# Kernel optimization log

Measured on AMD Instinct MI355X. Metric: run time of the kernel, lower is better.

The kernel has to match this reference:

```python
import jax, jax.numpy as jnp
import numpy as np

D = 1024      # in_dim
HS = 64       # head_size
H = 16        # num_heads
B, S = 2, 2048


def setup_inputs() -> dict:
    key = jax.random.key(0)
    k1, k2, k3, k4, k5, k6 = jax.random.split(key, 6)
    scale = 1.0 / np.sqrt(D)
    x = jax.random.normal(k1, (B, S, D), dtype=jnp.float32)
    # Stacked per-head projection weights (torch Linear weight is [out,in];
    # random init so layout only needs to be consistent). query weight exists
    # in the torch module but is never used (source bug), so it is omitted.
    Wk = jax.random.normal(k2, (H, D, HS), dtype=jnp.float32) * scale
    Wv = jax.random.normal(k3, (H, D, HS), dtype=jnp.float32) * scale
    Wproj = jax.random.normal(k4, (H * HS, D), dtype=jnp.float32) * (1.0 / np.sqrt(H * HS))
    bproj = jax.random.normal(k5, (D,), dtype=jnp.float32) * 0.01
    return {"x": x, "Wk": Wk, "Wv": Wv, "Wproj": Wproj, "bproj": bproj}


def reference(x, Wk, Wv, Wproj, bproj):
    # Faithful to source: k = key(x); q = value(x); v = value(x)  (q == v, no softmax)
    k = jnp.einsum("bsd,hde->bhse", x, Wk)   # [B,H,S,HS]
    v = jnp.einsum("bsd,hde->bhse", x, Wv)   # [B,H,S,HS]
    q = v
    inv_sqrt = jnp.asarray(HS, x.dtype) ** -0.5
    wei = jnp.einsum("bhse,bhte->bhst", q, k) * inv_sqrt  # [B,H,S,S], unnormalized
    out = jnp.einsum("bhst,bhte->bhse", wei, v)            # [B,H,S,HS]
    # concat heads: [B,S,H*HS]
    out = jnp.transpose(out, (0, 2, 1, 3)).reshape(x.shape[0], x.shape[1], H * HS)
    return out @ Wproj + bproj  # [B,S,D]
```

## Files before the change

kernel.cpp:

```cpp
#include <hip/hip_runtime.h>

#define B_ 2
#define S_ 2048
#define D_ 1024
#define H_ 16
#define HS_ 64
#define HD_ 1024
#define BS_ (B_*S_)
#define BK_ 128
#define BKO_ 128
#define TP_ 136

typedef __attribute__((ext_vector_type(8))) short short8_t;
typedef __attribute__((ext_vector_type(4))) float float4_t;

__device__ inline unsigned short f32_to_bf16(float f) {
  unsigned int u = __float_as_uint(f);
  u += 0x7FFF + ((u >> 16) & 1);
  return (unsigned short)(u >> 16);
}

__device__ inline void async_copy16(const void* g, void* lds) {
  __builtin_amdgcn_global_load_lds(
      (const __attribute__((address_space(1))) void*)g,
      (__attribute__((address_space(3))) void*)lds, 16, 0, 0);
}


__global__ __launch_bounds__(256) void prep_kernel(
    const float* __restrict__ x, const float* __restrict__ Wk,
    const float* __restrict__ Wv, unsigned short* __restrict__ xb,
    unsigned short* __restrict__ Wkvt) {
  const int blk = blockIdx.x;
  const int tid = threadIdx.x;
  __shared__ float lds[64][65];
  if (blk < 4096) {
    int idx = blk * 256 + tid;
    float4 v = ((const float4*)x)[idx];
    ushort4 o;
    o.x = f32_to_bf16(v.x); o.y = f32_to_bf16(v.y);
    o.z = f32_to_bf16(v.z); o.w = f32_to_bf16(v.w);
    ((ushort4*)xb)[idx] = o;
    return;
  }
  const int wblk = blk - 4096;
  const int h = wblk >> 4;
  const int d0 = (wblk & 15) * 64;
#pragma unroll
  for (int i = 0; i < 16; ++i) {
    int idx = tid + i * 256; int dd = idx >> 6, e = idx & 63;
    lds[e][dd] = Wk[((size_t)h * D_ + d0 + dd) * HS_ + e];
  }
  __syncthreads();
#pragma unroll
  for (int i = 0; i < 16; ++i) {
    int idx = tid + i * 256; int e = idx >> 6, dd = idx & 63;
    Wkvt[((size_t)h * 128 + e) * D_ + d0 + dd] = f32_to_bf16(lds[e][dd]);
  }
  __syncthreads();
#pragma unroll
  for (int i = 0; i < 16; ++i) {
    int idx = tid + i * 256; int dd = idx >> 6, e = idx & 63;
    lds[e][dd] = Wv[((size_t)h * D_ + d0 + dd) * HS_ + e];
  }
  __syncthreads();
#pragma unroll
  for (int i = 0; i < 16; ++i) {
    int idx = tid + i * 256; int e = idx >> 6, dd = idx & 63;
    Wkvt[((size_t)h * 128 + 64 + e) * D_ + d0 + dd] = f32_to_bf16(lds[e][dd]);
  }
}

__global__ __launch_bounds__(256) void kv_mfma_kernel(
    const unsigned short* __restrict__ xb,
    const unsigned short* __restrict__ Wkvt,
    unsigned short* __restrict__ Vb,
    float* __restrict__ Mpart) {
  const int blk = blockIdx.x;
  const int stile = blk & 31;
  const int h = blk >> 5;
  const int s0 = stile * 128;
  const int tid = threadIdx.x;
  const int lane = tid & 63;
  const int wid = tid >> 6;
  const int wm = wid & 1, wn = wid >> 1;
  const int quad = lane >> 4, l16 = lane & 15;
  const int srow4 = lane >> 4;
  const int xa = l16 & 7;

  __shared__ __align__(16) unsigned char smem[2 * 128 * BK_ * 2];
  unsigned short* As  = (unsigned short*)smem;
  unsigned short* Bs  = (unsigned short*)(smem + 128 * BK_ * 2);
  unsigned short* Ktl = (unsigned short*)smem;
  unsigned short* Vtl = (unsigned short*)(smem + 64 * TP_ * 2);

  float4_t acc[4][4];
  const float4_t fz = {0.f, 0.f, 0.f, 0.f};
#pragma unroll
  for (int i = 0; i < 4; ++i)
#pragma unroll
    for (int j = 0; j < 4; ++j) acc[i][j] = fz;

  for (int k0 = 0; k0 < D_; k0 += BK_) {
#pragma unroll
    for (int i = 0; i < 8; ++i) {
      int g = wid * 8 + i;
      int r = g * 4 + srow4;
      int ch = ((lane & 15) ^ (r & 7)) * 8;
      async_copy16(xb + (size_t)(s0 + r) * D_ + k0 + ch, As + g * 4 * BK_);
      async_copy16(Wkvt + ((size_t)h * 128 + r) * D_ + k0 + ch, Bs + g * 4 * BK_);
    }
    __syncthreads();
#pragma unroll
    for (int ks = 0; ks < 4; ++ks) {
      short8_t a[4], b[4];
#pragma unroll
      for (int mi = 0; mi < 4; ++mi)
        a[mi] = *(const short8_t*)(As + (wm * 64 + mi * 16 + l16) * BK_ +
                                   ((ks * 4 + quad) ^ xa) * 8);
#pragma unroll
      for (int ni = 0; ni < 4; ++ni)
        b[ni] = *(const short8_t*)(Bs + (wn * 64 + ni * 16 + l16) * BK_ +
                                   ((ks * 4 + quad) ^ xa) * 8);
#pragma unroll
      for (int mi = 0; mi < 4; ++mi)
#pragma unroll
        for (int ni = 0; ni < 4; ++ni)
          acc[mi][ni] = __builtin_amdgcn_mfma_f32_16x16x32_bf16(
              a[mi], b[ni], acc[mi][ni], 0, 0, 0);
    }
    __syncthreads();
  }

  {
    unsigned short* dstT = (wn == 0) ? Ktl : Vtl;
#pragma unroll
    for (int mi = 0; mi < 4; ++mi)
#pragma unroll
      for (int ni = 0; ni < 4; ++ni) {
        int f = ni * 16 + l16;
        int sm = wm * 64 + mi * 16 + quad * 4;
        ushort4 o;
        o.x = f32_to_bf16(acc[mi][ni][0]);
        o.y = f32_to_bf16(acc[mi][ni][1]);
        o.z = f32_to_bf16(acc[mi][ni][2]);
        o.w = f32_to_bf16(acc[mi][ni][3]);
        *(ushort4*)&dstT[f * TP_ + sm] = o;
      }
  }
  __syncthreads();

#pragma unroll
  for (int u = 0; u < 4; ++u) {
    int unit = tid + u * 256;
    int s = unit & 127;
    int ec = (unit >> 7) * 8;
    union { unsigned short u16[8]; uint4 v; } t;
#pragma unroll
    for (int e = 0; e < 8; ++e) t.u16[e] = Vtl[(ec + e) * TP_ + s];
    *(uint4*)&Vb[(size_t)(s0 + s) * HD_ + h * 64 + ec] = t.v;
  }

  {
    float4_t macc[4];
#pragma unroll
    for (int ni = 0; ni < 4; ++ni) macc[ni] = fz;
#pragma unroll
    for (int ss = 0; ss < 4; ++ss) {
      short8_t ka = *(const short8_t*)&Ktl[(wid * 16 + l16) * TP_ + ss * 32 + quad * 8];
#pragma unroll
      for (int ni = 0; ni < 4; ++ni) {
        short8_t vv = *(const short8_t*)&Vtl[(ni * 16 + l16) * TP_ + ss * 32 + quad * 8];
        macc[ni] = __builtin_amdgcn_mfma_f32_16x16x32_bf16(ka, vv, macc[ni], 0, 0, 0);
      }
    }
    float* mdst = Mpart + ((size_t)stile * H_ + h) * 4096;
#pragma unroll
    for (int ni = 0; ni < 4; ++ni) {
      int e = ni * 16 + l16;
#pragma unroll
      for (int r = 0; r < 4; ++r) {
        int f = wid * 16 + quad * 4 + r;
        mdst[f * 64 + e] = macc[ni][r];
      }
    }
  }
}

__global__ __launch_bounds__(256) void m_reduce_kernel(
    const float* __restrict__ Mpart, float* __restrict__ M) {
  const int gid = blockIdx.x * 256 + threadIdx.x;
  const int e0 = gid * 4;
  const int bh = e0 >> 12;
  const int idx = e0 & 4095;
  const int b = bh >> 4, h = bh & 15;
  float4 s = {0.f, 0.f, 0.f, 0.f};
#pragma unroll
  for (int p = 0; p < 16; ++p) {
    const float4 v =
        *(const float4*)&Mpart[(((size_t)(b * 16 + p)) * H_ + h) * 4096 + idx];
    s.x += v.x; s.y += v.y; s.z += v.z; s.w += v.w;
  }
  s.x *= 0.125f; s.y *= 0.125f; s.z *= 0.125f; s.w *= 0.125f;
  *(float4*)&M[(size_t)bh * 4096 + idx] = s;
}

__global__ __launch_bounds__(256) void p_kernel(
    const float* __restrict__ M, const float* __restrict__ Wproj,
    unsigned short* __restrict__ Pt) {
  const int blk = blockIdx.x;
  const int dtile = blk & 15;
  const int h = (blk >> 4) & 15;
  const int b = blk >> 8;
  const int d0 = dtile * 64;
  const int tid = threadIdx.x;
  const int tx = tid & 15, ty = tid >> 4;
  __shared__ float Ms[64][68];
  __shared__ float Ws[64][68];
  const size_t mbase = ((size_t)(b * H_ + h)) * HS_ * HS_;
#pragma unroll
  for (int i = 0; i < 16; ++i) {
    int idx = tid + i * 256;
    int f = idx >> 6, e = idx & 63;
    Ms[e][f] = M[mbase + idx];
    Ws[f][e] = Wproj[(size_t)(h * HS_ + f) * D_ + d0 + e];
  }
  __syncthreads();
  float acc[4][4] = {};
#pragma unroll
  for (int kk = 0; kk < 64; ++kk) {
    const float4 a4 = *(const float4*)&Ms[kk][ty * 4];
    const float4 b4 = *(const float4*)&Ws[kk][tx * 4];
    const float a[4] = {a4.x, a4.y, a4.z, a4.w};
    const float bb[4] = {b4.x, b4.y, b4.z, b4.w};
#pragma unroll
    for (int i = 0; i < 4; ++i)
#pragma unroll
      for (int j = 0; j < 4; ++j) acc[i][j] += a[i] * bb[j];
  }
  __syncthreads();
#pragma unroll
  for (int i = 0; i < 4; ++i)
#pragma unroll
    for (int j = 0; j < 4; ++j)
      Ms[tx * 4 + j][ty * 4 + i] = acc[i][j];
  __syncthreads();
  {
    int c = tid >> 2, ch = tid & 3;
    unsigned short* dst = Pt + ((size_t)(b * D_ + d0 + c)) * HD_ + h * 64 + ch * 16;
#pragma unroll
    for (int e = 0; e < 16; ++e) dst[e] = f32_to_bf16(Ms[c][ch * 16 + e]);
  }
}

__global__ __launch_bounds__(256) void out_mfma_kernel(
    const unsigned short* __restrict__ Vb,
    const unsigned short* __restrict__ Pt,
    const float* __restrict__ bproj,
    float* __restrict__ out) {
  const int blk = blockIdx.x;
  const int ntile = blk & 15;
  const int stile = blk >> 4;
  const int s0 = stile * 128;
  const int n0 = ntile * 64;
  const int b = s0 >> 11;
  const int tid = threadIdx.x;
  const int lane = tid & 63;
  const int wid = tid >> 6;
  const int wm = wid & 1, wn = wid >> 1;
  const int quad = lane >> 4, l16 = lane & 15;
  const int srow4 = lane >> 4;
  const int xa = l16 & 7;

  __shared__ __align__(16) unsigned short As[128 * BKO_];
  __shared__ __align__(16) unsigned short Bs[64 * BKO_];

  float4_t acc[4][2];
  const float4_t fz = {0.f, 0.f, 0.f, 0.f};
#pragma unroll
  for (int i = 0; i < 4; ++i)
#pragma unroll
    for (int j = 0; j < 2; ++j) acc[i][j] = fz;

  const unsigned short* Bpanel = Pt + (size_t)b * D_ * HD_;
  for (int k0 = 0; k0 < HD_; k0 += BKO_) {
#pragma unroll
    for (int i = 0; i < 8; ++i) {
      int g = wid * 8 + i;
      int r = g * 4 + srow4;
      int ch = ((lane & 15) ^ (r & 7)) * 8;
      async_copy16(Vb + (size_t)(s0 + r) * HD_ + k0 + ch, As + g * 4 * BKO_);
    }
#pragma unroll
    for (int i = 0; i < 4; ++i) {
      int g = wid * 4 + i;
      int r = g * 4 + srow4;
      int ch = ((lane & 15) ^ (r & 7)) * 8;
      async_copy16(Bpanel + (size_t)(n0 + r) * HD_ + k0 + ch, Bs + g * 4 * BKO_);
    }
    __syncthreads();
    short8_t a[4][4], bfr[2][4];
#pragma unroll
    for (int mi = 0; mi < 4; ++mi)
#pragma unroll
      for (int ks = 0; ks < 4; ++ks)
        a[mi][ks] = *(const short8_t*)(As + (wm * 64 + mi * 16 + l16) * BKO_ +
                                       ((ks * 4 + quad) ^ xa) * 8);
#pragma unroll
    for (int ni = 0; ni < 2; ++ni)
#pragma unroll
      for (int ks = 0; ks < 4; ++ks)
        bfr[ni][ks] = *(const short8_t*)(Bs + (wn * 32 + ni * 16 + l16) * BKO_ +
                                         ((ks * 4 + quad) ^ xa) * 8);
#pragma unroll
    for (int ks = 0; ks < 4; ++ks)
#pragma unroll
      for (int mi = 0; mi < 4; ++mi)
#pragma unroll
        for (int ni = 0; ni < 2; ++ni)
          acc[mi][ni] = __builtin_amdgcn_mfma_f32_16x16x32_bf16(
              a[mi][ks], bfr[ni][ks], acc[mi][ni], 0, 0, 0);
    __syncthreads();
  }
#pragma unroll
  for (int ni = 0; ni < 2; ++ni) {
    int col = n0 + wn * 32 + ni * 16 + l16;
    float bias = bproj[col];
#pragma unroll
    for (int mi = 0; mi < 4; ++mi) {
      int rowb = s0 + wm * 64 + mi * 16 + quad * 4;
#pragma unroll
      for (int r = 0; r < 4; ++r)
        out[(size_t)(rowb + r) * D_ + col] = acc[mi][ni][r] + bias;
    }
  }
}

extern "C" void kernel_launch(void* const* d_in, const int* in_sizes, int n_in,
                              void* d_out, int out_size, void* d_ws, size_t ws_size,
                              hipStream_t stream) {
  const float* x = (const float*)d_in[0];
  const float* Wk = (const float*)d_in[1];
  const float* Wv = (const float*)d_in[2];
  const float* Wproj = (const float*)d_in[3];
  const float* bproj = (const float*)d_in[4];
  float* out = (float*)d_out;

  char* ws = (char*)d_ws;
  unsigned short* xb = (unsigned short*)ws;
  unsigned short* Wkvt = xb + (size_t)BS_ * D_;
  unsigned short* Vb = Wkvt + (size_t)H_ * 128 * D_;
  float* Mpart = (float*)(Vb + (size_t)BS_ * HD_);
  float* M = Mpart + (size_t)32 * H_ * 4096;
  unsigned short* Pt = (unsigned short*)(M + (size_t)B_ * H_ * 4096);

  prep_kernel<<<dim3(4096 + H_ * (D_ / 64)), dim3(256), 0, stream>>>(x, Wk, Wv, xb, Wkvt);
  kv_mfma_kernel<<<dim3(32 * H_), dim3(256), 0, stream>>>(xb, Wkvt, Vb, Mpart);
  m_reduce_kernel<<<dim3(128), dim3(256), 0, stream>>>(Mpart, M);
  p_kernel<<<dim3(B_ * H_ * (D_ / 64)), dim3(256), 0, stream>>>(M, Wproj, Pt);
  out_mfma_kernel<<<dim3(32 * 16), dim3(256), 0, stream>>>(Vb, Pt, bproj, out);
}
```

Baseline: 132.1 us.

## Double-buffer LDS K-tiles with async prefetch in projection GEMM kernels

Both the KV projection and output projection GEMMs now use a two-stage LDS ping-pong with K-step 64 instead of a single buffer with K-step 128. The next tile's global_load_lds is issued before computing the current tile, using explicit vmcnt waits and raw barriers so loads overlap with MFMA work. s_setprio is raised around the MFMA blocks. This adds LDS usage (64KB in the KV kernel), which may cut occupancy, and relies on hand-counted vmcnt values being correct.

```diff
diff --git a/kernel.cpp b/kernel.cpp
--- a/kernel.cpp
+++ b/kernel.cpp
@@ -7,8 +7,7 @@
 #define HS_ 64
 #define HD_ 1024
 #define BS_ (B_*S_)
-#define BK_ 128
-#define BKO_ 128
+#define KS_ 64
 #define TP_ 136
 
 typedef __attribute__((ext_vector_type(8))) short short8_t;
@@ -85,12 +84,15 @@
   const int wid = tid >> 6;
   const int wm = wid & 1, wn = wid >> 1;
   const int quad = lane >> 4, l16 = lane & 15;
-  const int srow4 = lane >> 4;
+  const int srow8 = lane >> 3;
+  const int sc8 = lane & 7;
   const int xa = l16 & 7;
 
-  __shared__ __align__(16) unsigned char smem[2 * 128 * BK_ * 2];
-  unsigned short* As  = (unsigned short*)smem;
-  unsigned short* Bs  = (unsigned short*)(smem + 128 * BK_ * 2);
+  __shared__ __align__(16) unsigned char smem[65536];
+  unsigned short* const A0 = (unsigned short*)smem;
+  unsigned short* const B0 = (unsigned short*)(smem + 16384);
+  unsigned short* const A1 = (unsigned short*)(smem + 32768);
+  unsigned short* const B1 = (unsigned short*)(smem + 49152);
   unsigned short* Ktl = (unsigned short*)smem;
   unsigned short* Vtl = (unsigned short*)(smem + 64 * TP_ * 2);
 
@@ -101,35 +103,56 @@
 #pragma unroll
     for (int j = 0; j < 4; ++j) acc[i][j] = fz;
 
-  for (int k0 = 0; k0 < D_; k0 += BK_) {
-#pragma unroll
-    for (int i = 0; i < 8; ++i) {
-      int g = wid * 8 + i;
-      int r = g * 4 + srow4;
-      int ch = ((lane & 15) ^ (r & 7)) * 8;
-      async_copy16(xb + (size_t)(s0 + r) * D_ + k0 + ch, As + g * 4 * BK_);
-      async_copy16(Wkvt + ((size_t)h * 128 + r) * D_ + k0 + ch, Bs + g * 4 * BK_);
-    }
-    __syncthreads();
-#pragma unroll
-    for (int ks = 0; ks < 4; ++ks) {
+  auto stage = [&](int kt, unsigned short* Ad, unsigned short* Bd) {
+    const int k0 = kt * KS_;
+#pragma unroll
+    for (int i = 0; i < 4; ++i) {
+      int g = wid * 4 + i;
+      int r = g * 8 + srow8;
+      int ch = (sc8 ^ (r & 7)) * 8;
+      async_copy16(xb + (size_t)(s0 + r) * D_ + k0 + ch, Ad + g * 8 * KS_);
+      async_copy16(Wkvt + ((size_t)h * 128 + r) * D_ + k0 + ch, Bd + g * 8 * KS_);
+    }
+  };
+  auto compute = [&](const unsigned short* Ac, const unsigned short* Bc) {
+#pragma unroll
+    for (int ks = 0; ks < 2; ++ks) {
       short8_t a[4], b[4];
 #pragma unroll
       for (int mi = 0; mi < 4; ++mi)
-        a[mi] = *(const short8_t*)(As + (wm * 64 + mi * 16 + l16) * BK_ +
+        a[mi] = *(const short8_t*)(Ac + (wm * 64 + mi * 16 + l16) * KS_ +
                                    ((ks * 4 + quad) ^ xa) * 8);
 #pragma unroll
       for (int ni = 0; ni < 4; ++ni)
-        b[ni] = *(const short8_t*)(Bs + (wn * 64 + ni * 16 + l16) * BK_ +
+        b[ni] = *(const short8_t*)(Bc + (wn * 64 + ni * 16 + l16) * KS_ +
                                    ((ks * 4 + quad) ^ xa) * 8);
+      __builtin_amdgcn_s_setprio(1);
 #pragma unroll
       for (int mi = 0; mi < 4; ++mi)
 #pragma unroll
         for (int ni = 0; ni < 4; ++ni)
           acc[mi][ni] = __builtin_amdgcn_mfma_f32_16x16x32_bf16(
               a[mi], b[ni], acc[mi][ni], 0, 0, 0);
-    }
-    __syncthreads();
+      __builtin_amdgcn_s_setprio(0);
+    }
+  };
+
+  stage(0, A0, B0);
+#pragma unroll
+  for (int t = 0; t < 16; ++t) {
+    unsigned short* Ac = (t & 1) ? A1 : A0;
+    unsigned short* Bc = (t & 1) ? B1 : B0;
+    if (t < 15) {
+      stage(t + 1, (t & 1) ? A0 : A1, (t & 1) ? B0 : B1);
+      asm volatile("s_waitcnt vmcnt(8)" ::: "memory");
+    } else {
+      asm volatile("s_waitcnt vmcnt(0)" ::: "memory");
+    }
+    __builtin_amdgcn_s_barrier();
+    __builtin_amdgcn_sched_barrier(0);
+    compute(Ac, Bc);
+    __builtin_amdgcn_sched_barrier(0);
+    __builtin_amdgcn_s_barrier();
   }
 
   {
@@ -269,11 +292,15 @@
   const int wid = tid >> 6;
   const int wm = wid & 1, wn = wid >> 1;
   const int quad = lane >> 4, l16 = lane & 15;
-  const int srow4 = lane >> 4;
+  const int srow8 = lane >> 3;
+  const int sc8 = lane & 7;
   const int xa = l16 & 7;
 
-  __shared__ __align__(16) unsigned short As[128 * BKO_];
-  __shared__ __align__(16) unsigned short Bs[64 * BKO_];
+  __shared__ __align__(16) unsigned char smem[49152];
+  unsigned short* const A0 = (unsigned short*)smem;
+  unsigned short* const B0 = (unsigned short*)(smem + 16384);
+  unsigned short* const A1 = (unsigned short*)(smem + 24576);
+  unsigned short* const B1 = (unsigned short*)(smem + 40960);
 
   float4_t acc[4][2];
   const float4_t fz = {0.f, 0.f, 0.f, 0.f};
@@ -283,45 +310,64 @@
     for (int j = 0; j < 2; ++j) acc[i][j] = fz;
 
   const unsigned short* Bpanel = Pt + (size_t)b * D_ * HD_;
-  for (int k0 = 0; k0 < HD_; k0 += BKO_) {
-#pragma unroll
-    for (int i = 0; i < 8; ++i) {
-      int g = wid * 8 + i;
-      int r = g * 4 + srow4;
-      int ch = ((lane & 15) ^ (r & 7)) * 8;
-      async_copy16(Vb + (size_t)(s0 + r) * HD_ + k0 + ch, As + g * 4 * BKO_);
-    }
+  auto stage = [&](int kt, unsigned short* Ad, unsigned short* Bd) {
+    const int k0 = kt * KS_;
 #pragma unroll
     for (int i = 0; i < 4; ++i) {
       int g = wid * 4 + i;
-      int r = g * 4 + srow4;
-      int ch = ((lane & 15) ^ (r & 7)) * 8;
-      async_copy16(Bpanel + (size_t)(n0 + r) * HD_ + k0 + ch, Bs + g * 4 * BKO_);
-    }
-    __syncthreads();
-    short8_t a[4][4], bfr[2][4];
-#pragma unroll
-    for (int mi = 0; mi < 4; ++mi)
-#pragma unroll
-      for (int ks = 0; ks < 4; ++ks)
-        a[mi][ks] = *(const short8_t*)(As + (wm * 64 + mi * 16 + l16) * BKO_ +
-                                       ((ks * 4 + quad) ^ xa) * 8);
-#pragma unroll
-    for (int ni = 0; ni < 2; ++ni)
-#pragma unroll
-      for (int ks = 0; ks < 4; ++ks)
-        bfr[ni][ks] = *(const short8_t*)(Bs + (wn * 32 + ni * 16 + l16) * BKO_ +
-                                         ((ks * 4 + quad) ^ xa) * 8);
-#pragma unroll
-    for (int ks = 0; ks < 4; ++ks)
+      int r = g * 8 + srow8;
+      int ch = (sc8 ^ (r & 7)) * 8;
+      async_copy16(Vb + (size_t)(s0 + r) * HD_ + k0 + ch, Ad + g * 8 * KS_);
+    }
+#pragma unroll
+    for (int i = 0; i < 2; ++i) {
+      int g = wid * 2 + i;
+      int r = g * 8 + srow8;
+      int ch = (sc8 ^ (r & 7)) * 8;
+      async_copy16(Bpanel + (size_t)(n0 + r) * HD_ + k0 + ch, Bd + g * 8 * KS_);
+    }
+  };
+  auto compute = [&](const unsigned short* Ac, const unsigned short* Bc) {
+#pragma unroll
+    for (int ks = 0; ks < 2; ++ks) {
+      short8_t a[4], bfr[2];
+#pragma unroll
+      for (int mi = 0; mi < 4; ++mi)
+        a[mi] = *(const short8_t*)(Ac + (wm * 64 + mi * 16 + l16) * KS_ +
+                                   ((ks * 4 + quad) ^ xa) * 8);
+#pragma unroll
+      for (int ni = 0; ni < 2; ++ni)
+        bfr[ni] = *(const short8_t*)(Bc + (wn * 32 + ni * 16 + l16) * KS_ +
+                                     ((ks * 4 + quad) ^ xa) * 8);
+      __builtin_amdgcn_s_setprio(1);
 #pragma unroll
       for (int mi = 0; mi < 4; ++mi)
 #pragma unroll
         for (int ni = 0; ni < 2; ++ni)
           acc[mi][ni] = __builtin_amdgcn_mfma_f32_16x16x32_bf16(
-              a[mi][ks], bfr[ni][ks], acc[mi][ni], 0, 0, 0);
-    __syncthreads();
-  }
+              a[mi], bfr[ni], acc[mi][ni], 0, 0, 0);
+      __builtin_amdgcn_s_setprio(0);
+    }
+  };
+
+  stage(0, A0, B0);
+#pragma unroll
+  for (int t = 0; t < 16; ++t) {
+    unsigned short* Ac = (t & 1) ? A1 : A0;
+    unsigned short* Bc = (t & 1) ? B1 : B0;
+    if (t < 15) {
+      stage(t + 1, (t & 1) ? A0 : A1, (t & 1) ? B0 : B1);
+      asm volatile("s_waitcnt vmcnt(6)" ::: "memory");
+    } else {
+      asm volatile("s_waitcnt vmcnt(0)" ::: "memory");
+    }
+    __builtin_amdgcn_s_barrier();
+    __builtin_amdgcn_sched_barrier(0);
+    compute(Ac, Bc);
+    __builtin_amdgcn_sched_barrier(0);
+    __builtin_amdgcn_s_barrier();
+  }
+
 #pragma unroll
   for (int ni = 0; ni < 2; ++ni) {
     int col = n0 + wn * 32 + ni * 16 + l16;
```

New measurement: 128.4 us. 1.03x faster.
